# Optimization experiments

Hardware: AMD Instinct MI355X
Metric: run time of the kernel (lower is better)

## Reference

```python
import jax, jax.numpy as jnp
import numpy as np

FIXED_SIZE = (160, 160, 160)

def _reference_grid(grid_size):
    # [d1, d2, d3, 3] float32 grid of voxel indices, as in layer_util.get_reference_grid
    ax = [jnp.arange(d, dtype=jnp.float32) for d in grid_size]
    return jnp.stack(jnp.meshgrid(*ax, indexing="ij"), axis=-1)

def _resample_linear(vol, loc):
    # vol: [B, D1, D2, D3]; loc: [B, f1, f2, f3, 3] (voxel coords in vol space)
    B = vol.shape[0]
    dims = vol.shape[1:4]
    max_f = jnp.asarray([d - 1 for d in dims], dtype=loc.dtype)
    max_i = jnp.asarray([d - 1 for d in dims], dtype=jnp.int32)
    locc = jnp.clip(loc, 0.0, max_f)          # clamp to volume bounds
    lo = jnp.floor(locc)
    w = locc - lo                              # trilinear weights in [0,1]
    i0 = lo.astype(jnp.int32)
    i1 = jnp.minimum(i0 + 1, max_i)
    b = jnp.arange(B).reshape(B, 1, 1, 1)
    x0, y0, z0 = i0[..., 0], i0[..., 1], i0[..., 2]
    x1, y1, z1 = i1[..., 0], i1[..., 1], i1[..., 2]
    wx, wy, wz = w[..., 0], w[..., 1], w[..., 2]
    ux, uy, uz = 1.0 - wx, 1.0 - wy, 1.0 - wz
    g = lambda ix, iy, iz: vol[b, ix, iy, iz]  # 8-neighbor gather
    return (g(x0, y0, z0) * ux * uy * uz +
            g(x0, y0, z1) * ux * uy * wz +
            g(x0, y1, z0) * ux * wy * uz +
            g(x0, y1, z1) * ux * wy * wz +
            g(x1, y0, z0) * wx * uy * uz +
            g(x1, y0, z1) * wx * uy * wz +
            g(x1, y1, z0) * wx * wy * uz +
            g(x1, y1, z1) * wx * wy * wz)

def setup_inputs() -> dict:
    key = jax.random.key(0)
    k1, k2 = jax.random.split(key)
    B = 4
    ddf = jax.random.normal(k1, (B,) + FIXED_SIZE + (3,), dtype=jnp.float32)
    image = jax.random.normal(k2, (B,) + FIXED_SIZE, dtype=jnp.float32)
    return {"ddf": ddf, "image": image}

def reference(ddf, image):
    grid_ref = _reference_grid(FIXED_SIZE)[None]      # [1, f1, f2, f3, 3]
    grid_warped = grid_ref + ddf                      # [B, f1, f2, f3, 3]
    return _resample_linear(image, grid_warped)       # [B, f1, f2, f3]
```

## Files before the change

### kernel.cpp

```cpp
#include <hip/hip_runtime.h>

#define D     160
#define D2    (D * D)
#define D3    (D * D * D)
#define NB    4
#define TL    4
#define ZSL   32
#define ZWIN  40
#define WINX  12
#define RING  24
#define PLANE 480
#define LDSF  (RING * PLANE)
#define TPB   256
#define NWAVE 4
#define TPDX  (D / TL)
#define TPDZ  (D / ZSL)
#define CNT   10
#define NRUN  4
#define NBLK  (NB * TPDX * TPDZ * NRUN)

typedef float f32x2 __attribute__((ext_vector_type(2)));
typedef int   i32x2 __attribute__((ext_vector_type(2)));

struct AState {
    f32x2 wx2, wy2, wz2;
    int ba[2], bc[2];
    unsigned flags, shb;
    f32x2 fb00[2], fb01[2], fb10[2], fb11[2];
};

__device__ __forceinline__ void phaseA(
    const float* __restrict__ vol,
    float xgf, float ygf, float zgf,
    int xwb, int ywb, int zwb, int su,
    f32x2 q0, f32x2 q1, f32x2 q2, AState& S)
{
    const f32x2 zero2 = {0.0f, 0.0f};
    const f32x2 max2  = {(float)(D - 1), (float)(D - 1)};
    f32x2 dx = {q0.x, q1.y};
    f32x2 dy = {q0.y, q2.x};
    f32x2 dz = {q1.x, q2.y};
    f32x2 xg2 = {xgf, xgf};
    f32x2 yg2 = {ygf, ygf};
    f32x2 zg2 = {zgf, zgf + 1.0f};

    f32x2 fx2 = __builtin_elementwise_min(
                    __builtin_elementwise_max(xg2 + dx, zero2), max2);
    f32x2 fy2 = __builtin_elementwise_min(
                    __builtin_elementwise_max(yg2 + dy, zero2), max2);
    f32x2 fz2 = __builtin_elementwise_min(
                    __builtin_elementwise_max(zg2 + dz, zero2), max2);

    i32x2 X0 = __builtin_convertvector(fx2, i32x2);
    i32x2 Y0 = __builtin_convertvector(fy2, i32x2);
    i32x2 Z0 = __builtin_convertvector(fz2, i32x2);
    S.wx2 = fx2 - __builtin_convertvector(X0, f32x2);
    S.wy2 = fy2 - __builtin_convertvector(Y0, f32x2);
    S.wz2 = fz2 - __builtin_convertvector(Z0, f32x2);

    S.flags = 0; S.shb = 0;
#pragma unroll
    for (int j = 0; j < 2; ++j) {
        S.fb00[j] = f32x2{0, 0}; S.fb01[j] = f32x2{0, 0};
        S.fb10[j] = f32x2{0, 0}; S.fb11[j] = f32x2{0, 0};
        int x0 = X0[j], y0 = Y0[j], z0 = Z0[j];
        int sx0 = x0 - xwb, sy0 = y0 - ywb, sz0 = z0 - zwb;
        bool inWin = ((unsigned)sx0 <= 10u) & ((unsigned)sy0 <= 10u) &
                     ((unsigned)sz0 <= 38u);
        S.flags |= (unsigned)inWin << j;
        int csx = min(max(sx0, 0), 10);
        int csy = min(max(sy0, 0), 10);
        int csz = min(max(sz0, 0), 38);
        int t0 = su + csy; if (t0 >= RING) t0 -= RING;
        int t1 = t0 + 1;   if (t1 == RING) t1 = 0;
        S.ba[j] = t0 * PLANE + csx * ZWIN + csz;
        S.bc[j] = t1 * PLANE + csx * ZWIN + csz;
        if (!inWin) {
            int x1 = min(x0 + 1, D - 1);
            int y1 = min(y0 + 1, D - 1);
            int zc = min(z0, D - 2);
            S.shb |= (unsigned)(z0 > zc) << j;
            S.fb00[j] = *(const f32x2*)(vol + x0 * D2 + y0 * D + zc);
            S.fb01[j] = *(const f32x2*)(vol + x0 * D2 + y1 * D + zc);
            S.fb10[j] = *(const f32x2*)(vol + x1 * D2 + y0 * D + zc);
            S.fb11[j] = *(const f32x2*)(vol + x1 * D2 + y1 * D + zc);
        }
    }
}

__device__ __forceinline__ f32x2 phaseB(const float* __restrict__ buf,
                                        const AState& S)
{
    const f32x2 one2 = {1.0f, 1.0f};
    float a0s[2], a1s[2], c0s[2], c1s[2], e0s[2], e1s[2], g0s[2], g1s[2];
#pragma unroll
    for (int j = 0; j < 2; ++j) {
        a0s[j] = buf[S.ba[j]];          a1s[j] = buf[S.ba[j] + 1];
        c0s[j] = buf[S.bc[j]];          c1s[j] = buf[S.bc[j] + 1];
        e0s[j] = buf[S.ba[j] + ZWIN];   e1s[j] = buf[S.ba[j] + ZWIN + 1];
        g0s[j] = buf[S.bc[j] + ZWIN];   g1s[j] = buf[S.bc[j] + ZWIN + 1];
        if (!((S.flags >> j) & 1)) {
            bool sh = (S.shb >> j) & 1;
            a0s[j] = sh ? S.fb00[j].y : S.fb00[j].x;  a1s[j] = S.fb00[j].y;
            c0s[j] = sh ? S.fb01[j].y : S.fb01[j].x;  c1s[j] = S.fb01[j].y;
            e0s[j] = sh ? S.fb10[j].y : S.fb10[j].x;  e1s[j] = S.fb10[j].y;
            g0s[j] = sh ? S.fb11[j].y : S.fb11[j].x;  g1s[j] = S.fb11[j].y;
        }
    }
    f32x2 A0 = {a0s[0], a0s[1]}, A1 = {a1s[0], a1s[1]};
    f32x2 C0 = {c0s[0], c0s[1]}, C1 = {c1s[0], c1s[1]};
    f32x2 E0 = {e0s[0], e0s[1]}, E1 = {e1s[0], e1s[1]};
    f32x2 G0 = {g0s[0], g0s[1]}, G1 = {g1s[0], g1s[1]};

    f32x2 ux2 = one2 - S.wx2, uy2 = one2 - S.wy2, uz2 = one2 - S.wz2;
    return (A0 * uz2 + A1 * S.wz2) * (ux2 * uy2)
         + (C0 * uz2 + C1 * S.wz2) * (ux2 * S.wy2)
         + (E0 * uz2 + E1 * S.wz2) * (S.wx2 * uy2)
         + (G0 * uz2 + G1 * S.wz2) * (S.wx2 * S.wy2);
}

__global__ __launch_bounds__(TPB) void warp_kernel(
    const float* __restrict__ ddf,
    const float* __restrict__ image,
    float* __restrict__ out)
{
    extern __shared__ float buf[];

    const int tid  = threadIdx.x;
    const int w    = tid >> 6;
    const int lane = tid & 63;
    const int row  = tid >> 4;
    const int zch  = tid & 15;
    const int rx   = row >> 2, ry = row & 3, zbl = zch * 2;

    int g    = blockIdx.x;
    int gx8  = (g & 7) * (NBLK / 8) + (g >> 3);
    int yrun = gx8 & 3;
    int t    = gx8 >> 2;
    int zi   = t % TPDZ;  t /= TPDZ;
    int xi   = t % TPDX;
    int b    = t / TPDX;

    const int yt0    = yrun * (CNT * TL);
    const int xt     = xi * TL, zl = zi * ZSL;
    const int xwb    = xt - 4,  zwb = zl - 4;
    const int volofs = b * D3;
    const float* vol = image + volofs;

    int pfix[2];
#pragma unroll
    for (int k = 0; k < 2; ++k) {
        int f  = k * 256 + lane * 4;
        int sx = f / ZWIN;
        int zo = f - sx * ZWIN;
        int srcx = min(max(xwb + sx, 0), D - 1);
        int srcz = min(max(zwb + zo, 0), D - 4);
        pfix[k] = volofs + srcx * D2 + srcz;
    }

    int su = yt0 % RING;

    int   vb  = volofs + (xt + rx) * D2 + (yt0 + ry) * D + (zl + zbl);
    float ygf = (float)(yt0 + ry);
    const float xgf = (float)(xt + rx);
    const float zgf = (float)(zl + zbl);
    int   ywb = yt0 - 4;

#pragma unroll
    for (int m = 0; m < 8; ++m) {
        int L  = w + m * NWAVE;
        int pi = L >> 1, k = L & 1;
        int p  = yt0 - 4 + pi;
        int srcy = max(p, 0);
        int slot = su + pi; if (slot >= RING) slot -= RING;
        if (k == 0 || lane < 56) {
            const float* gp = image + pfix[k] + srcy * D;
            __builtin_amdgcn_global_load_lds(
                (const __attribute__((address_space(1))) void*)gp,
                (__attribute__((address_space(3))) void*)(buf + slot * PLANE + k * 256),
                16, 0, 0);
        }
    }
    f32x2 qa0, qa1, qa2, qb0, qb1, qb2;
    f32x2 na0 = {0,0}, na1 = {0,0}, na2 = {0,0};
    f32x2 nb0 = {0,0}, nb1 = {0,0}, nb2 = {0,0};
    {
        const float* p = ddf + (size_t)vb * 3;
        qa0 = __builtin_nontemporal_load((const f32x2*)p);
        qa1 = __builtin_nontemporal_load((const f32x2*)(p + 2));
        qa2 = __builtin_nontemporal_load((const f32x2*)(p + 4));
        const float* p2 = ddf + (size_t)(vb + TL * D) * 3;
        qb0 = __builtin_nontemporal_load((const f32x2*)p2);
        qb1 = __builtin_nontemporal_load((const f32x2*)(p2 + 2));
        qb2 = __builtin_nontemporal_load((const f32x2*)(p2 + 4));
    }
    asm volatile("s_waitcnt vmcnt(0)" ::: "memory");
    __builtin_amdgcn_sched_barrier(0);
    __builtin_amdgcn_s_barrier();
    __builtin_amdgcn_sched_barrier(0);

#pragma unroll 1
    for (int d = 0; d < 5; ++d) {
        const bool more = (d < 4);

        int su4 = su + 4; if (su4 >= RING) su4 -= RING;
        AState Sa, Sb;
        phaseA(vol, xgf, ygf,        zgf, xwb, ywb,     zwb, su,  qa0, qa1, qa2, Sa);
        phaseA(vol, xgf, ygf + 4.0f, zgf, xwb, ywb + 4, zwb, su4, qb0, qb1, qb2, Sb);
        __builtin_amdgcn_sched_barrier(0);

        if (more) {
            int ptop = ywb + 16;
            int ps   = su + 16; if (ps >= RING) ps -= RING;
#pragma unroll
            for (int s = 0; s < 4; ++s) {
                int L  = w + s * NWAVE;
                int pi = L >> 1, k = L & 1;
                int p  = ptop + pi;
                int srcy = min(p, D - 1);
                int slot = ps + pi; if (slot >= RING) slot -= RING;
                if (k == 0 || lane < 56) {
                    const float* gp = image + pfix[k] + srcy * D;
                    __builtin_amdgcn_global_load_lds(
                        (const __attribute__((address_space(1))) void*)gp,
                        (__attribute__((address_space(3))) void*)(buf + slot * PLANE + k * 256),
                        16, 0, 0);
                }
            }
        }
        __builtin_amdgcn_sched_barrier(0);

        if (more) {
            const float* p = ddf + (size_t)(vb + 8 * D) * 3;
            na0 = __builtin_nontemporal_load((const f32x2*)p);
            na1 = __builtin_nontemporal_load((const f32x2*)(p + 2));
            na2 = __builtin_nontemporal_load((const f32x2*)(p + 4));
            const float* p2 = ddf + (size_t)(vb + 12 * D) * 3;
            nb0 = __builtin_nontemporal_load((const f32x2*)p2);
            nb1 = __builtin_nontemporal_load((const f32x2*)(p2 + 2));
            nb2 = __builtin_nontemporal_load((const f32x2*)(p2 + 4));
        }
        __builtin_amdgcn_sched_barrier(0);

        f32x2 ra = phaseB(buf, Sa);
        f32x2 rb = phaseB(buf, Sb);
        __builtin_nontemporal_store(ra, (f32x2*)(out + vb));
        __builtin_nontemporal_store(rb, (f32x2*)(out + vb + 4 * D));
        __builtin_amdgcn_sched_barrier(0);

        if (more) {
            asm volatile("s_waitcnt vmcnt(8)" ::: "memory");
            __builtin_amdgcn_sched_barrier(0);
            __builtin_amdgcn_s_barrier();
            __builtin_amdgcn_sched_barrier(0);

            qa0 = na0; qa1 = na1; qa2 = na2;
            qb0 = nb0; qb1 = nb1; qb2 = nb2;
            vb += 8 * D; ygf += 8.0f; ywb += 8;
            su += 8; if (su >= RING) su -= RING;
        }
    }
}

extern "C" void kernel_launch(void* const* d_in, const int* in_sizes, int n_in,
                              void* d_out, int out_size, void* d_ws, size_t ws_size,
                              hipStream_t stream) {
    const float* ddf   = (const float*)d_in[0];
    const float* image = (const float*)d_in[1];
    float* out = (float*)d_out;

    warp_kernel<<<NBLK, TPB, LDSF * sizeof(float), stream>>>(ddf, image, out);
}
```

Before: 87.53 us.

## Shrink LDS plane ring and split image prefetch into two staged batches

Reduces the LDS ring buffer from 24 to 20 y-planes, lowering shared memory per block so more blocks can fit per CU. The image plane prefetch is split in two: one batch is issued before phase A and another after the ddf loads, each covering half the new planes per wave with a fixed k per wave. An extra barrier with a vmcnt wait is added before phase B, and the wait counts change accordingly. This trades an additional block-wide barrier per iteration for lower LDS footprint and earlier issue of part of the prefetch.

```diff
diff --git a/kernel.cpp b/kernel.cpp
--- a/kernel.cpp
+++ b/kernel.cpp
@@ -8,14 +8,13 @@
 #define ZSL   32
 #define ZWIN  40
 #define WINX  12
-#define RING  24
+#define RING  20
 #define PLANE 480
 #define LDSF  (RING * PLANE)
 #define TPB   256
 #define NWAVE 4
 #define TPDX  (D / TL)
 #define TPDZ  (D / ZSL)
-#define CNT   10
 #define NRUN  4
 #define NBLK  (NB * TPDX * TPDZ * NRUN)
 
@@ -141,7 +140,7 @@
     int xi   = t % TPDX;
     int b    = t / TPDX;
 
-    const int yt0    = yrun * (CNT * TL);
+    const int yt0    = yrun * 40;
     const int xt     = xi * TL, zl = zi * ZSL;
     const int xwb    = xt - 4,  zwb = zl - 4;
     const int volofs = b * D3;
@@ -158,21 +157,23 @@
         pfix[k] = volofs + srcx * D2 + srcz;
     }
 
-    int su = yt0 % RING;
+    int su = 0;
+    int ywb = yt0 - 4;
 
     int   vb  = volofs + (xt + rx) * D2 + (yt0 + ry) * D + (zl + zbl);
     float ygf = (float)(yt0 + ry);
     const float xgf = (float)(xt + rx);
     const float zgf = (float)(zl + zbl);
-    int   ywb = yt0 - 4;
-
-#pragma unroll
-    for (int m = 0; m < 8; ++m) {
+
+    const int kk = w & 1;
+
+#pragma unroll
+    for (int m = 0; m < 6; ++m) {
         int L  = w + m * NWAVE;
         int pi = L >> 1, k = L & 1;
-        int p  = yt0 - 4 + pi;
+        int p  = ywb + pi;
         int srcy = max(p, 0);
-        int slot = su + pi; if (slot >= RING) slot -= RING;
+        int slot = pi;
         if (k == 0 || lane < 56) {
             const float* gp = image + pfix[k] + srcy * D;
             __builtin_amdgcn_global_load_lds(
@@ -203,31 +204,29 @@
     for (int d = 0; d < 5; ++d) {
         const bool more = (d < 4);
 
+        {
+            int ps = su + 12; if (ps >= RING) ps -= RING;
+#pragma unroll
+            for (int s = 0; s < 2; ++s) {
+                int pi = (w >> 1) + s * 2;
+                int p  = ywb + 12 + pi;
+                int srcy = min(max(p, 0), D - 1);
+                int slot = ps + pi; if (slot >= RING) slot -= RING;
+                if (kk == 0 || lane < 56) {
+                    const float* gp = image + pfix[kk] + srcy * D;
+                    __builtin_amdgcn_global_load_lds(
+                        (const __attribute__((address_space(1))) void*)gp,
+                        (__attribute__((address_space(3))) void*)(buf + slot * PLANE + kk * 256),
+                        16, 0, 0);
+                }
+            }
+        }
+        __builtin_amdgcn_sched_barrier(0);
+
         int su4 = su + 4; if (su4 >= RING) su4 -= RING;
         AState Sa, Sb;
         phaseA(vol, xgf, ygf,        zgf, xwb, ywb,     zwb, su,  qa0, qa1, qa2, Sa);
         phaseA(vol, xgf, ygf + 4.0f, zgf, xwb, ywb + 4, zwb, su4, qb0, qb1, qb2, Sb);
-        __builtin_amdgcn_sched_barrier(0);
-
-        if (more) {
-            int ptop = ywb + 16;
-            int ps   = su + 16; if (ps >= RING) ps -= RING;
-#pragma unroll
-            for (int s = 0; s < 4; ++s) {
-                int L  = w + s * NWAVE;
-                int pi = L >> 1, k = L & 1;
-                int p  = ptop + pi;
-                int srcy = min(p, D - 1);
-                int slot = ps + pi; if (slot >= RING) slot -= RING;
-                if (k == 0 || lane < 56) {
-                    const float* gp = image + pfix[k] + srcy * D;
-                    __builtin_amdgcn_global_load_lds(
-                        (const __attribute__((address_space(1))) void*)gp,
-                        (__attribute__((address_space(3))) void*)(buf + slot * PLANE + k * 256),
-                        16, 0, 0);
-                }
-            }
-        }
         __builtin_amdgcn_sched_barrier(0);
 
         if (more) {
@@ -239,7 +238,29 @@
             nb0 = __builtin_nontemporal_load((const f32x2*)p2);
             nb1 = __builtin_nontemporal_load((const f32x2*)(p2 + 2));
             nb2 = __builtin_nontemporal_load((const f32x2*)(p2 + 4));
-        }
+            __builtin_amdgcn_sched_barrier(0);
+            int ps = su + 16; if (ps >= RING) ps -= RING;
+#pragma unroll
+            for (int s = 0; s < 2; ++s) {
+                int pi = (w >> 1) + s * 2;
+                int p  = ywb + 16 + pi;
+                int srcy = min(max(p, 0), D - 1);
+                int slot = ps + pi; if (slot >= RING) slot -= RING;
+                if (kk == 0 || lane < 56) {
+                    const float* gp = image + pfix[kk] + srcy * D;
+                    __builtin_amdgcn_global_load_lds(
+                        (const __attribute__((address_space(1))) void*)gp,
+                        (__attribute__((address_space(3))) void*)(buf + slot * PLANE + kk * 256),
+                        16, 0, 0);
+                }
+            }
+        }
+        __builtin_amdgcn_sched_barrier(0);
+
+        if (more) { asm volatile("s_waitcnt vmcnt(8)" ::: "memory"); }
+        else      { asm volatile("s_waitcnt vmcnt(0)" ::: "memory"); }
+        __builtin_amdgcn_sched_barrier(0);
+        __builtin_amdgcn_s_barrier();
         __builtin_amdgcn_sched_barrier(0);
 
         f32x2 ra = phaseB(buf, Sa);
@@ -249,7 +270,7 @@
         __builtin_amdgcn_sched_barrier(0);
 
         if (more) {
-            asm volatile("s_waitcnt vmcnt(8)" ::: "memory");
+            asm volatile("s_waitcnt vmcnt(4)" ::: "memory");
             __builtin_amdgcn_sched_barrier(0);
             __builtin_amdgcn_s_barrier();
             __builtin_amdgcn_sched_barrier(0);
```

Result: faster. 83.96 us (-4.1%).
